# Performance work log

Hardware: AMD Instinct MI355X
Metric: run time of the kernel (lower is better)

Reference implementation:

```python
import jax, jax.numpy as jnp
import numpy as np

B, C, H, W = 16, 1024, 32, 32


def setup_inputs() -> dict:
    key = jax.random.key(0)
    ka, kb, kc = jax.random.split(key, 3)
    a = jax.random.normal(ka, (B, C, H, W), dtype=jnp.float32)
    b = jax.random.normal(kb, (B, C, H, W), dtype=jnp.float32)
    c = jax.random.normal(kc, (B, C, H, W), dtype=jnp.float32)
    return {"a": a, "b": b, "c": c}


def reference(a, b, c):
    Bn, Cn = a.shape[0], a.shape[1]
    a_f = a.reshape(Bn, Cn, -1)  # [B, C, HW]
    b_f = b.reshape(Bn, Cn, -1)
    c_f = c.reshape(Bn, Cn, -1)
    # channel-attention scores: [B, C, C]
    scores = jnp.einsum('bik,bjk->bij', b_f, c_f)
    mid = jax.nn.softmax(scores, axis=-1)
    out = jnp.einsum('bij,bjk->bik', mid, a_f)  # [B, C, HW]
    out = out.reshape(a.shape) + a  # residual add
    return out
```

## Files before the change

kernel.cpp:

```cpp
#include <hip/hip_runtime.h>
#include <hip/hip_bf16.h>
#include <stdint.h>

#define BATCH 16
#define CDIM 1024
#define HWDIM 1024
#define PSTRIDE 2048

typedef _Float16 half_t;
typedef _Float16 half8 __attribute__((ext_vector_type(8)));
typedef float floatx4 __attribute__((ext_vector_type(4)));

__device__ static inline void gld_lds16(const half_t* g, half_t* l) {
    __builtin_amdgcn_global_load_lds(
        (__attribute__((address_space(1))) void*)(void*)g,
        (__attribute__((address_space(3))) void*)l, 16, 0, 0);
}

__global__ __launch_bounds__(256) void k_prep(const float* __restrict__ Bm,
                                              const float* __restrict__ Cm,
                                              half_t* __restrict__ dst) {
    const size_t N = (size_t)BATCH * CDIM * HWDIM;
    const float* src = blockIdx.y ? Cm : Bm;
    half_t* d = dst + (size_t)blockIdx.y * N;
    const size_t base = ((size_t)blockIdx.x * 256 + threadIdx.x) * 8;
    float4 f0 = *(const float4*)(src + base);
    float4 f1 = *(const float4*)(src + base + 4);
    half_t h[8];
    h[0] = (half_t)f0.x; h[1] = (half_t)f0.y; h[2] = (half_t)f0.z; h[3] = (half_t)f0.w;
    h[4] = (half_t)f1.x; h[5] = (half_t)f1.y; h[6] = (half_t)f1.z; h[7] = (half_t)f1.w;
    *(uint4*)(d + base) = *(const uint4*)h;
}

__global__ __launch_bounds__(256) void k_gemm1(const half_t* __restrict__ Bh,
                                               const half_t* __restrict__ Ch,
                                               float* __restrict__ S) {
    const int bz = blockIdx.z;
    const int i0 = blockIdx.x * 128;
    const int j0 = blockIdx.y * 128;
    const half_t* Ap = Bh + (size_t)bz * CDIM * HWDIM;
    const half_t* Bp = Ch + (size_t)bz * CDIM * HWDIM;
    float* Sp = S + (size_t)bz * CDIM * CDIM;

    __shared__ half_t lA[128 * 32];
    __shared__ half_t lB[128 * 32];

    const int tid = threadIdx.x;
    const int lane = tid & 63;
    const int wave = tid >> 6;
    const int wm = wave >> 1, wn = wave & 1;

    floatx4 acc[4][4];
#pragma unroll
    for (int a = 0; a < 4; ++a)
#pragma unroll
        for (int b = 0; b < 4; ++b) acc[a][b] = (floatx4){0.f, 0.f, 0.f, 0.f};

    const int srow = tid >> 2;
    const int scol = (tid & 3) * 8;
    const int fr = lane & 15;
    const int fk = (lane >> 4) * 8;

    for (int k0 = 0; k0 < HWDIM; k0 += 32) {
#pragma unroll
        for (int p = 0; p < 2; ++p) {
            gld_lds16(Ap + (size_t)(i0 + p * 64 + srow) * HWDIM + k0 + scol,
                      &lA[(p * 64 + srow) * 32 + scol]);
            gld_lds16(Bp + (size_t)(j0 + p * 64 + srow) * HWDIM + k0 + scol,
                      &lB[(p * 64 + srow) * 32 + scol]);
        }
        __syncthreads();
        half8 af[4], bfr[4];
#pragma unroll
        for (int mt = 0; mt < 4; ++mt)
            af[mt] = *(const half8*)&lA[(wm * 64 + mt * 16 + fr) * 32 + fk];
#pragma unroll
        for (int nt = 0; nt < 4; ++nt)
            bfr[nt] = *(const half8*)&lB[(wn * 64 + nt * 16 + fr) * 32 + fk];
#pragma unroll
        for (int mt = 0; mt < 4; ++mt)
#pragma unroll
            for (int nt = 0; nt < 4; ++nt)
                acc[mt][nt] = __builtin_amdgcn_mfma_f32_16x16x32_f16(
                    af[mt], bfr[nt], acc[mt][nt], 0, 0, 0);
        __syncthreads();
    }

    const int er = (lane >> 4) * 4;
    const int ec = lane & 15;
#pragma unroll
    for (int mt = 0; mt < 4; ++mt)
#pragma unroll
        for (int nt = 0; nt < 4; ++nt) {
            const int row = i0 + wm * 64 + mt * 16 + er;
            const int col = j0 + wn * 64 + nt * 16 + ec;
            float* dst = Sp + (size_t)row * CDIM + col;
#pragma unroll
            for (int r = 0; r < 4; ++r) dst[(size_t)r * CDIM] = acc[mt][nt][r];
        }
}

__global__ __launch_bounds__(256) void k_softmax(float* __restrict__ S) {
    float* rp = S + (size_t)blockIdx.x * CDIM;
    const int tid = threadIdx.x;
    float4 v = ((const float4*)rp)[tid];

    __shared__ float red[256];
    float m = fmaxf(fmaxf(v.x, v.y), fmaxf(v.z, v.w));
    red[tid] = m;
    __syncthreads();
    for (int s = 128; s > 0; s >>= 1) {
        if (tid < s) red[tid] = fmaxf(red[tid], red[tid + s]);
        __syncthreads();
    }
    m = red[0];
    __syncthreads();

    float e0 = __expf(v.x - m), e1 = __expf(v.y - m);
    float e2 = __expf(v.z - m), e3 = __expf(v.w - m);
    red[tid] = e0 + e1 + e2 + e3;
    __syncthreads();
    for (int s = 128; s > 0; s >>= 1) {
        if (tid < s) red[tid] += red[tid + s];
        __syncthreads();
    }
    const float inv = 1.0f / red[0];

    half_t p[4];
    p[0] = (half_t)(e0 * inv);
    p[1] = (half_t)(e1 * inv);
    p[2] = (half_t)(e2 * inv);
    p[3] = (half_t)(e3 * inv);
    ((uint2*)rp)[tid] = *(const uint2*)p;
}

__global__ __launch_bounds__(256) void k_transpose(const float* __restrict__ A,
                                                   half_t* __restrict__ SP) {
    const int bz = blockIdx.z;
    const int t0 = blockIdx.x * 64;
    const int j0 = blockIdx.y * 64;
    const float* Ap = A + (size_t)bz * CDIM * HWDIM;
    half_t* Atp = SP + (size_t)bz * CDIM * PSTRIDE + 1024;

    __shared__ half_t tile[64][68];
    const int lr = threadIdx.x >> 4;
    const int lc = (threadIdx.x & 15) * 4;
#pragma unroll
    for (int r = 0; r < 4; ++r) {
        const float* src = Ap + (size_t)(j0 + lr + r * 16) * HWDIM + t0 + lc;
        float4 f = *(const float4*)src;
        half_t t4[4];
        t4[0] = (half_t)f.x; t4[1] = (half_t)f.y;
        t4[2] = (half_t)f.z; t4[3] = (half_t)f.w;
        *(uint2*)&tile[lr + r * 16][lc] = *(const uint2*)t4;
    }
    __syncthreads();
#pragma unroll
    for (int r = 0; r < 4; ++r) {
        const int trow = lr + r * 16;
        half_t tmp[4];
#pragma unroll
        for (int e = 0; e < 4; ++e) tmp[e] = tile[lc + e][trow];
        *(uint2*)(Atp + (size_t)(t0 + trow) * PSTRIDE + j0 + lc) = *(uint2*)tmp;
    }
}

__global__ __launch_bounds__(256) void k_gemm2(const half_t* __restrict__ SP,
                                               const float* __restrict__ Aorig,
                                               float* __restrict__ Out) {
    const int bz = blockIdx.z;
    const int i0 = blockIdx.x * 128;
    const int t0 = blockIdx.y * 128;
    const half_t* Pp = SP + (size_t)bz * CDIM * PSTRIDE;
    const half_t* Bp = SP + (size_t)bz * CDIM * PSTRIDE + 1024;

    __shared__ half_t lA[128 * 32];
    __shared__ half_t lB[128 * 32];

    const int tid = threadIdx.x;
    const int lane = tid & 63;
    const int wave = tid >> 6;
    const int wm = wave >> 1, wn = wave & 1;

    floatx4 acc[4][4];
#pragma unroll
    for (int a = 0; a < 4; ++a)
#pragma unroll
        for (int b = 0; b < 4; ++b) acc[a][b] = (floatx4){0.f, 0.f, 0.f, 0.f};

    const int srow = tid >> 2;
    const int scol = (tid & 3) * 8;
    const int fr = lane & 15;
    const int fk = (lane >> 4) * 8;

    for (int k0 = 0; k0 < CDIM; k0 += 32) {
#pragma unroll
        for (int p = 0; p < 2; ++p) {
            gld_lds16(Pp + (size_t)(i0 + p * 64 + srow) * PSTRIDE + k0 + scol,
                      &lA[(p * 64 + srow) * 32 + scol]);
            gld_lds16(Bp + (size_t)(t0 + p * 64 + srow) * PSTRIDE + k0 + scol,
                      &lB[(p * 64 + srow) * 32 + scol]);
        }
        __syncthreads();
        half8 af[4], bfr[4];
#pragma unroll
        for (int mt = 0; mt < 4; ++mt)
            af[mt] = *(const half8*)&lA[(wm * 64 + mt * 16 + fr) * 32 + fk];
#pragma unroll
        for (int nt = 0; nt < 4; ++nt)
            bfr[nt] = *(const half8*)&lB[(wn * 64 + nt * 16 + fr) * 32 + fk];
#pragma unroll
        for (int mt = 0; mt < 4; ++mt)
#pragma unroll
            for (int nt = 0; nt < 4; ++nt)
                acc[mt][nt] = __builtin_amdgcn_mfma_f32_16x16x32_f16(
                    af[mt], bfr[nt], acc[mt][nt], 0, 0, 0);
        __syncthreads();
    }

    const float* ap = Aorig + (size_t)bz * CDIM * HWDIM;
    float* op = Out + (size_t)bz * CDIM * HWDIM;
    const int er = (lane >> 4) * 4;
    const int ec = lane & 15;
#pragma unroll
    for (int mt = 0; mt < 4; ++mt)
#pragma unroll
        for (int nt = 0; nt < 4; ++nt) {
            const int col = t0 + wn * 64 + nt * 16 + ec;
#pragma unroll
            for (int r = 0; r < 4; ++r) {
                const int row = i0 + wm * 64 + mt * 16 + er + r;
                const size_t idx = (size_t)row * HWDIM + col;
                op[idx] = acc[mt][nt][r] + ap[idx];
            }
        }
}

extern "C" void kernel_launch(void* const* d_in, const int* in_sizes, int n_in,
                              void* d_out, int out_size, void* d_ws, size_t ws_size,
                              hipStream_t stream) {
    const float* a = (const float*)d_in[0];
    const float* b = (const float*)d_in[1];
    const float* c = (const float*)d_in[2];
    float* out = (float*)d_out;

    float* S = (float*)d_ws;
    half_t* bc16 = (half_t*)d_out;

    k_prep<<<dim3(8192, 2), 256, 0, stream>>>(b, c, bc16);
    k_gemm1<<<dim3(8, 8, 16), 256, 0, stream>>>(
        bc16, bc16 + (size_t)BATCH * CDIM * HWDIM, S);
    k_softmax<<<dim3(BATCH * CDIM), 256, 0, stream>>>(S);
    k_transpose<<<dim3(16, 16, 16), 256, 0, stream>>>(a, (half_t*)S);
    k_gemm2<<<dim3(8, 8, 16), 256, 0, stream>>>((const half_t*)S, a, out);
}
```

Baseline: 355.9 us.

## Rewrite both GEMMs with 256x256 tiles and double-buffered swizzled LDS pipeline

Both batched GEMMs now share one device routine that computes 256x256 output tiles with 512 threads. It stages 64-wide K slices into double-buffered, XOR-swizzled LDS via global_load_lds, and interleaves the loads with MFMA phases using explicit waitcnt, barriers and setprio. Block indices are remapped so that neighbouring tiles spread across compute dies. The aim is to raise arithmetic intensity, hide global-load latency and avoid LDS bank conflicts, which the old synchronous 128x128, K=32 loop could not do. The cost is 128KB of LDS per block, so only one block fits per CU, plus a heavy accumulator register footprint.

```diff
diff --git a/kernel.cpp b/kernel.cpp
--- a/kernel.cpp
+++ b/kernel.cpp
@@ -6,6 +6,8 @@
 #define CDIM 1024
 #define HWDIM 1024
 #define PSTRIDE 2048
+#define TILE_E (256 * 64)
+#define NTK 16
 
 typedef _Float16 half_t;
 typedef _Float16 half8 __attribute__((ext_vector_type(8)));
@@ -15,6 +17,145 @@
     __builtin_amdgcn_global_load_lds(
         (__attribute__((address_space(1))) void*)(void*)g,
         (__attribute__((address_space(3))) void*)l, 16, 0, 0);
+}
+
+__device__ __forceinline__ half8 ld8(const char* p) { return *(const half8*)p; }
+
+template <int MB, int NB>
+__device__ __forceinline__ void mfma16(floatx4 (&acc)[8][4],
+                                       const half8 (&a4)[4][2],
+                                       const half8 (&b2)[2][2]) {
+#pragma unroll
+    for (int mt = 0; mt < 4; ++mt)
+#pragma unroll
+        for (int nt = 0; nt < 2; ++nt)
+#pragma unroll
+            for (int ks = 0; ks < 2; ++ks)
+                acc[MB + mt][NB + nt] = __builtin_amdgcn_mfma_f32_16x16x32_f16(
+                    a4[mt][ks], b2[nt][ks], acc[MB + mt][NB + nt], 0, 0, 0);
+}
+
+__device__ __forceinline__ void gemm8p(const half_t* __restrict__ Ag, size_t sA,
+                                       const half_t* __restrict__ Bg, size_t sB,
+                                       int i0, int j0,
+                                       half_t* lA, half_t* lB,
+                                       floatx4 (&acc)[8][4]) {
+    const int tid = threadIdx.x;
+    const int lane = tid & 63;
+    const int wave = tid >> 6;
+    const int wm = wave >> 2, wn = wave & 3;
+    const int fr = lane & 15, hi = lane >> 4;
+    const int sw = (fr & 7) << 4;
+    const int o0 = fr * 128 + ((hi * 16) ^ sw);
+    const int o1 = fr * 128 + ((hi * 16 + 64) ^ sw);
+
+    const int r0 = tid >> 3;
+    const int scol = ((tid & 7) ^ (r0 & 7)) * 8;
+    const half_t* pa = Ag + (size_t)(i0 + r0) * sA + scol;
+    const half_t* pb = Bg + (size_t)(j0 + r0) * sB + scol;
+
+#pragma unroll
+    for (int a = 0; a < 8; ++a)
+#pragma unroll
+        for (int b = 0; b < 4; ++b) acc[a][b] = (floatx4){0.f, 0.f, 0.f, 0.f};
+
+#define STG_A(tt, h)                                                      \
+    do {                                                                  \
+        const half_t* g_ = pa + (size_t)(h) * 128 * sA + (tt) * 64;       \
+        half_t* l_ = lA + ((tt) & 1) * TILE_E + (h) * 8192 + tid * 8;     \
+        gld_lds16(g_, l_);                                                \
+        gld_lds16(g_ + 64 * sA, l_ + 4096);                               \
+    } while (0)
+#define STG_B(tt, h)                                                      \
+    do {                                                                  \
+        const half_t* g_ = pb + (size_t)(h) * 128 * sB + (tt) * 64;       \
+        half_t* l_ = lB + ((tt) & 1) * TILE_E + (h) * 8192 + tid * 8;     \
+        gld_lds16(g_, l_);                                                \
+        gld_lds16(g_ + 64 * sB, l_ + 4096);                               \
+    } while (0)
+
+    STG_A(0, 0); STG_B(0, 0); STG_A(0, 1); STG_B(0, 1);
+    STG_B(1, 0); STG_A(1, 0); STG_B(1, 1);
+    asm volatile("s_waitcnt vmcnt(6)" ::: "memory");
+    __builtin_amdgcn_s_barrier();
+
+    half8 af[4][2], bf0[2][2], bf1[2][2];
+
+#pragma unroll 2
+    for (int t = 0; t < NTK; ++t) {
+        const char* aw = (const char*)(lA + (t & 1) * TILE_E) + wm * 8192;
+        const char* bw = (const char*)(lB + (t & 1) * TILE_E) + wn * 4096;
+
+#pragma unroll
+        for (int mt = 0; mt < 4; ++mt) {
+            af[mt][0] = ld8(aw + mt * 2048 + o0);
+            af[mt][1] = ld8(aw + mt * 2048 + o1);
+        }
+#pragma unroll
+        for (int nt = 0; nt < 2; ++nt) {
+            bf0[nt][0] = ld8(bw + nt * 2048 + o0);
+            bf0[nt][1] = ld8(bw + nt * 2048 + o1);
+        }
+        if (t + 1 < NTK) STG_A(t + 1, 1);
+        __builtin_amdgcn_s_barrier();
+        asm volatile("s_waitcnt lgkmcnt(0)" ::: "memory");
+        __builtin_amdgcn_s_setprio(1);
+        mfma16<0, 0>(acc, af, bf0);
+        __builtin_amdgcn_s_setprio(0);
+        __builtin_amdgcn_sched_barrier(0);
+        __builtin_amdgcn_s_barrier();
+
+#pragma unroll
+        for (int nt = 0; nt < 2; ++nt) {
+            bf1[nt][0] = ld8(bw + 16384 + nt * 2048 + o0);
+            bf1[nt][1] = ld8(bw + 16384 + nt * 2048 + o1);
+        }
+        if (t + 2 < NTK) STG_B(t + 2, 0);
+        __builtin_amdgcn_s_barrier();
+        asm volatile("s_waitcnt lgkmcnt(0)" ::: "memory");
+        __builtin_amdgcn_s_setprio(1);
+        mfma16<0, 2>(acc, af, bf1);
+        __builtin_amdgcn_s_setprio(0);
+        __builtin_amdgcn_sched_barrier(0);
+        __builtin_amdgcn_s_barrier();
+
+#pragma unroll
+        for (int mt = 0; mt < 4; ++mt) {
+            af[mt][0] = ld8(aw + 16384 + mt * 2048 + o0);
+            af[mt][1] = ld8(aw + 16384 + mt * 2048 + o1);
+        }
+        if (t + 2 < NTK) STG_A(t + 2, 0);
+        __builtin_amdgcn_s_barrier();
+        asm volatile("s_waitcnt lgkmcnt(0)" ::: "memory");
+        __builtin_amdgcn_s_setprio(1);
+        mfma16<4, 2>(acc, af, bf1);
+        __builtin_amdgcn_s_setprio(0);
+        __builtin_amdgcn_sched_barrier(0);
+        __builtin_amdgcn_s_barrier();
+
+        if (t + 2 < NTK) STG_B(t + 2, 1);
+        if (t < NTK - 2)
+            asm volatile("s_waitcnt vmcnt(6)" ::: "memory");
+        else
+            asm volatile("s_waitcnt vmcnt(0)" ::: "memory");
+        __builtin_amdgcn_s_barrier();
+        __builtin_amdgcn_s_setprio(1);
+        mfma16<4, 0>(acc, af, bf0);
+        __builtin_amdgcn_s_setprio(0);
+        __builtin_amdgcn_sched_barrier(0);
+        __builtin_amdgcn_s_barrier();
+    }
+#undef STG_A
+#undef STG_B
+}
+
+__device__ __forceinline__ void tile_coords(int& bz, int& i0, int& j0) {
+    const int flat = blockIdx.x + (blockIdx.y << 4);
+    const int w = ((flat & 7) << 5) + (flat >> 3);
+    bz = w >> 4;
+    const int tl = w & 15;
+    i0 = (tl & 3) << 8;
+    j0 = (tl >> 2) << 8;
 }
 
 __global__ __launch_bounds__(256) void k_prep(const float* __restrict__ Bm,
@@ -32,72 +173,35 @@
     *(uint4*)(d + base) = *(const uint4*)h;
 }
 
-__global__ __launch_bounds__(256) void k_gemm1(const half_t* __restrict__ Bh,
-                                               const half_t* __restrict__ Ch,
-                                               float* __restrict__ S) {
-    const int bz = blockIdx.z;
-    const int i0 = blockIdx.x * 128;
-    const int j0 = blockIdx.y * 128;
-    const half_t* Ap = Bh + (size_t)bz * CDIM * HWDIM;
-    const half_t* Bp = Ch + (size_t)bz * CDIM * HWDIM;
+__global__ __launch_bounds__(512, 2) void k_gemm1(const half_t* __restrict__ Bh,
+                                                  const half_t* __restrict__ Ch,
+                                                  float* __restrict__ S) {
+    __shared__ half_t lA[2 * TILE_E];
+    __shared__ half_t lB[2 * TILE_E];
+    int bz, i0, j0;
+    tile_coords(bz, i0, j0);
+
+    floatx4 acc[8][4];
+    gemm8p(Bh + (size_t)bz * CDIM * HWDIM, HWDIM,
+           Ch + (size_t)bz * CDIM * HWDIM, HWDIM, i0, j0, lA, lB, acc);
+
     float* Sp = S + (size_t)bz * CDIM * CDIM;
-
-    __shared__ half_t lA[128 * 32];
-    __shared__ half_t lB[128 * 32];
-
-    const int tid = threadIdx.x;
-    const int lane = tid & 63;
-    const int wave = tid >> 6;
-    const int wm = wave >> 1, wn = wave & 1;
-
-    floatx4 acc[4][4];
-#pragma unroll
-    for (int a = 0; a < 4; ++a)
-#pragma unroll
-        for (int b = 0; b < 4; ++b) acc[a][b] = (floatx4){0.f, 0.f, 0.f, 0.f};
-
-    const int srow = tid >> 2;
-    const int scol = (tid & 3) * 8;
-    const int fr = lane & 15;
-    const int fk = (lane >> 4) * 8;
-
-    for (int k0 = 0; k0 < HWDIM; k0 += 32) {
-#pragma unroll
-        for (int p = 0; p < 2; ++p) {
-            gld_lds16(Ap + (size_t)(i0 + p * 64 + srow) * HWDIM + k0 + scol,
-                      &lA[(p * 64 + srow) * 32 + scol]);
-            gld_lds16(Bp + (size_t)(j0 + p * 64 + srow) * HWDIM + k0 + scol,
-                      &lB[(p * 64 + srow) * 32 + scol]);
-        }
-        __syncthreads();
-        half8 af[4], bfr[4];
-#pragma unroll
-        for (int mt = 0; mt < 4; ++mt)
-            af[mt] = *(const half8*)&lA[(wm * 64 + mt * 16 + fr) * 32 + fk];
-#pragma unroll
-        for (int nt = 0; nt < 4; ++nt)
-            bfr[nt] = *(const half8*)&lB[(wn * 64 + nt * 16 + fr) * 32 + fk];
-#pragma unroll
-        for (int mt = 0; mt < 4; ++mt)
-#pragma unroll
-            for (int nt = 0; nt < 4; ++nt)
-                acc[mt][nt] = __builtin_amdgcn_mfma_f32_16x16x32_f16(
-                    af[mt], bfr[nt], acc[mt][nt], 0, 0, 0);
-        __syncthreads();
-    }
-
+    const int lane = threadIdx.x & 63;
+    const int wave = threadIdx.x >> 6;
+    const int wm = wave >> 2, wn = wave & 3;
     const int er = (lane >> 4) * 4;
     const int ec = lane & 15;
 #pragma unroll
-    for (int mt = 0; mt < 4; ++mt)
+    for (int mt = 0; mt < 8; ++mt) {
+        const int row0 = i0 + ((mt >> 2) << 7) + wm * 64 + (mt & 3) * 16 + er;
 #pragma unroll
         for (int nt = 0; nt < 4; ++nt) {
-            const int row = i0 + wm * 64 + mt * 16 + er;
-            const int col = j0 + wn * 64 + nt * 16 + ec;
-            float* dst = Sp + (size_t)row * CDIM + col;
+            const int col = j0 + ((nt >> 1) << 7) + wn * 32 + (nt & 1) * 16 + ec;
+            float* dst = Sp + (size_t)row0 * CDIM + col;
 #pragma unroll
             for (int r = 0; r < 4; ++r) dst[(size_t)r * CDIM] = acc[mt][nt][r];
         }
+    }
 }
 
 __global__ __launch_bounds__(256) void k_softmax(float* __restrict__ S) {
@@ -165,75 +269,40 @@
     }
 }
 
-__global__ __launch_bounds__(256) void k_gemm2(const half_t* __restrict__ SP,
-                                               const float* __restrict__ Aorig,
-                                               float* __restrict__ Out) {
-    const int bz = blockIdx.z;
-    const int i0 = blockIdx.x * 128;
-    const int t0 = blockIdx.y * 128;
+__global__ __launch_bounds__(512, 2) void k_gemm2(const half_t* __restrict__ SP,
+                                                  const float* __restrict__ Aorig,
+                                                  float* __restrict__ Out) {
+    __shared__ half_t lA[2 * TILE_E];
+    __shared__ half_t lB[2 * TILE_E];
+    int bz, i0, t0;
+    tile_coords(bz, i0, t0);
+
     const half_t* Pp = SP + (size_t)bz * CDIM * PSTRIDE;
-    const half_t* Bp = SP + (size_t)bz * CDIM * PSTRIDE + 1024;
-
-    __shared__ half_t lA[128 * 32];
-    __shared__ half_t lB[128 * 32];
-
-    const int tid = threadIdx.x;
-    const int lane = tid & 63;
-    const int wave = tid >> 6;
-    const int wm = wave >> 1, wn = wave & 1;
-
-    floatx4 acc[4][4];
-#pragma unroll
-    for (int a = 0; a < 4; ++a)
-#pragma unroll
-        for (int b = 0; b < 4; ++b) acc[a][b] = (floatx4){0.f, 0.f, 0.f, 0.f};
-
-    const int srow = tid >> 2;
-    const int scol = (tid & 3) * 8;
-    const int fr = lane & 15;
-    const int fk = (lane >> 4) * 8;
-
-    for (int k0 = 0; k0 < CDIM; k0 += 32) {
-#pragma unroll
-        for (int p = 0; p < 2; ++p) {
-            gld_lds16(Pp + (size_t)(i0 + p * 64 + srow) * PSTRIDE + k0 + scol,
-                      &lA[(p * 64 + srow) * 32 + scol]);
-            gld_lds16(Bp + (size_t)(t0 + p * 64 + srow) * PSTRIDE + k0 + scol,
-                      &lB[(p * 64 + srow) * 32 + scol]);
-        }
-        __syncthreads();
-        half8 af[4], bfr[4];
-#pragma unroll
-        for (int mt = 0; mt < 4; ++mt)
-            af[mt] = *(const half8*)&lA[(wm * 64 + mt * 16 + fr) * 32 + fk];
-#pragma unroll
-        for (int nt = 0; nt < 4; ++nt)
-            bfr[nt] = *(const half8*)&lB[(wn * 64 + nt * 16 + fr) * 32 + fk];
-#pragma unroll
-        for (int mt = 0; mt < 4; ++mt)
-#pragma unroll
-            for (int nt = 0; nt < 4; ++nt)
-                acc[mt][nt] = __builtin_amdgcn_mfma_f32_16x16x32_f16(
-                    af[mt], bfr[nt], acc[mt][nt], 0, 0, 0);
-        __syncthreads();
-    }
+    const half_t* Bp = Pp + 1024;
+
+    floatx4 acc[8][4];
+    gemm8p(Pp, PSTRIDE, Bp, PSTRIDE, i0, t0, lA, lB, acc);
 
     const float* ap = Aorig + (size_t)bz * CDIM * HWDIM;
     float* op = Out + (size_t)bz * CDIM * HWDIM;
+    const int lane = threadIdx.x & 63;
+    const int wave = threadIdx.x >> 6;
+    const int wm = wave >> 2, wn = wave & 3;
     const int er = (lane >> 4) * 4;
     const int ec = lane & 15;
 #pragma unroll
-    for (int mt = 0; mt < 4; ++mt)
+    for (int mt = 0; mt < 8; ++mt) {
+        const int row0 = i0 + ((mt >> 2) << 7) + wm * 64 + (mt & 3) * 16 + er;
 #pragma unroll
         for (int nt = 0; nt < 4; ++nt) {
-            const int col = t0 + wn * 64 + nt * 16 + ec;
+            const int col = t0 + ((nt >> 1) << 7) + wn * 32 + (nt & 1) * 16 + ec;
 #pragma unroll
             for (int r = 0; r < 4; ++r) {
-                const int row = i0 + wm * 64 + mt * 16 + er + r;
-                const size_t idx = (size_t)row * HWDIM + col;
+                const size_t idx = (size_t)(row0 + r) * HWDIM + col;
                 op[idx] = acc[mt][nt][r] + ap[idx];
             }
         }
+    }
 }
 
 extern "C" void kernel_launch(void* const* d_in, const int* in_sizes, int n_in,
@@ -248,9 +317,9 @@
     half_t* bc16 = (half_t*)d_out;
 
     k_prep<<<dim3(8192, 2), 256, 0, stream>>>(b, c, bc16);
-    k_gemm1<<<dim3(8, 8, 16), 256, 0, stream>>>(
+    k_gemm1<<<dim3(16, 16), 512, 0, stream>>>(
         bc16, bc16 + (size_t)BATCH * CDIM * HWDIM, S);
     k_softmax<<<dim3(BATCH * CDIM), 256, 0, stream>>>(S);
     k_transpose<<<dim3(16, 16, 16), 256, 0, stream>>>(a, (half_t*)S);
-    k_gemm2<<<dim3(8, 8, 16), 256, 0, stream>>>((const half_t*)S, a, out);
-}
+    k_gemm2<<<dim3(16, 16), 512, 0, stream>>>((const half_t*)S, a, out);
+}
```

Result: faster. 315.4 us (-11.4%).
